# Kernel optimization log

Hardware: AMD Instinct MI355X
Metric: run time of the kernel (lower is better)

## Reference

```python
import jax, jax.numpy as jnp
import numpy as np

N_NODES = 100000
N_EDGES = 1600000
IN_FEATS = 16
HIDDEN = 100
OUT_FEATS = 3


def setup_inputs() -> dict:
    key = jax.random.key(0)
    ks = jax.random.split(key, 12)
    inp = {
        "x": jax.random.normal(ks[0], (N_NODES, IN_FEATS), dtype=jnp.float32),
        "edge_feats": jax.random.uniform(ks[1], (N_EDGES, 1), dtype=jnp.float32),
        "src": jax.random.randint(ks[2], (N_EDGES,), 0, N_NODES, dtype=jnp.int32),
        "dst": jax.random.randint(ks[3], (N_EDGES,), 0, N_NODES, dtype=jnp.int32),
        # lift: Linear(in_feats, hidden)
        "W_lift": jax.random.normal(ks[4], (IN_FEATS, HIDDEN), dtype=jnp.float32) / np.sqrt(IN_FEATS),
        "b_lift": jnp.zeros((HIDDEN,), dtype=jnp.float32),
        # three MPL layers: Linear(2*hidden, hidden)
        "W1": jax.random.normal(ks[5], (2 * HIDDEN, HIDDEN), dtype=jnp.float32) / np.sqrt(2 * HIDDEN),
        "b1": jnp.zeros((HIDDEN,), dtype=jnp.float32),
        "W2": jax.random.normal(ks[6], (2 * HIDDEN, HIDDEN), dtype=jnp.float32) / np.sqrt(2 * HIDDEN),
        "b2": jnp.zeros((HIDDEN,), dtype=jnp.float32),
        "W3": jax.random.normal(ks[7], (2 * HIDDEN, HIDDEN), dtype=jnp.float32) / np.sqrt(2 * HIDDEN),
        "b3": jnp.zeros((HIDDEN,), dtype=jnp.float32),
        # out: Linear(hidden, out_feats)
        "W_out": jax.random.normal(ks[8], (HIDDEN, OUT_FEATS), dtype=jnp.float32) / np.sqrt(HIDDEN),
        "b_out": jnp.zeros((OUT_FEATS,), dtype=jnp.float32),
    }
    return inp


def _mpl(h, edge_feats, src, dst, W, b):
    # gather src node feats, multiply by per-edge weight, scatter-sum to dst
    msg = h[src] * edge_feats                                # [E, H]
    reduced = jax.ops.segment_sum(msg, dst, num_segments=N_NODES)  # [N, H]
    return jax.nn.relu(jnp.concatenate([h, reduced], axis=-1) @ W + b)


def reference(x, edge_feats, src, dst, W_lift, b_lift, W1, b1, W2, b2, W3, b3, W_out, b_out):
    h = jnp.tanh(x @ W_lift + b_lift)          # [N, 100]
    h = _mpl(h, edge_feats, src, dst, W1, b1)
    h = _mpl(h, edge_feats, src, dst, W2, b2)
    h = _mpl(h, edge_feats, src, dst, W3, b3)
    return jax.nn.sigmoid(h @ W_out + b_out)   # [N, 3]
```

## Files before the change

kernel.cpp:

```cpp
#include <hip/hip_runtime.h>
#include <hip/hip_fp16.h>
#include <cstdint>
#include <cstddef>

#define NN 100000
#define NE 1600000
#define HID 100
#define INF 16

typedef _Float16 f16x8 __attribute__((ext_vector_type(8)));
typedef float f32x4 __attribute__((ext_vector_type(4)));

__device__ __forceinline__ float2 up_f16(unsigned int u) {
  __half2 h = *reinterpret_cast<const __half2*>(&u);
  return __half22float2(h);
}
__device__ __forceinline__ unsigned int pk_f16(float lo, float hi) {
  __half2 h = __floats2half2_rn(lo, hi);
  return *reinterpret_cast<const unsigned int*>(&h);
}
__device__ __forceinline__ f16x8 as_f16x8(uint4 v) {
  union { uint4 u; f16x8 f; } c; c.u = v; return c.f;
}

__global__ void k_hist(const int* __restrict__ dst, int* __restrict__ deg,
                       int* __restrict__ rank) {
  int e = blockIdx.x * 256 + threadIdx.x;
  if (e < NE) rank[e] = atomicAdd(&deg[dst[e]], 1);
}

__global__ void k_scan1(const int* __restrict__ deg, int* __restrict__ offs,
                        int* __restrict__ bsum) {
  __shared__ int s[256];
  int t = threadIdx.x;
  int i = blockIdx.x * 256 + t;
  int v = (i < NN) ? deg[i] : 0;
  s[t] = v; __syncthreads();
  for (int off = 1; off < 256; off <<= 1) {
    int x = (t >= off) ? s[t - off] : 0;
    __syncthreads();
    s[t] += x;
    __syncthreads();
  }
  if (i < NN) offs[i] = s[t] - v;
  if (t == 255) bsum[blockIdx.x] = s[255];
}

__global__ void k_scan2(int* __restrict__ bsum, int nb) {
  __shared__ int s[512];
  int t = threadIdx.x;
  int v = (t < nb) ? bsum[t] : 0;
  s[t] = v; __syncthreads();
  for (int off = 1; off < 512; off <<= 1) {
    int x = (t >= off) ? s[t - off] : 0;
    __syncthreads();
    s[t] += x;
    __syncthreads();
  }
  if (t < nb) bsum[t] = s[t] - v;
}

__global__ void k_scan3(int* __restrict__ offs, const int* __restrict__ bsum) {
  int i = blockIdx.x * 256 + threadIdx.x;
  if (i < NN) offs[i] += bsum[i >> 8];
  else if (i == NN) offs[NN] = NE;
}

__global__ void k_fill(const int* __restrict__ src, const int* __restrict__ dst,
                       const float* __restrict__ ef, const int* __restrict__ offs,
                       const int* __restrict__ rank,
                       unsigned long long* __restrict__ epack) {
  int e = blockIdx.x * 256 + threadIdx.x;
  if (e >= NE) return;
  int p = offs[dst[e]] + rank[e];
  unsigned long long v = (unsigned int)src[e] |
                         ((unsigned long long)(unsigned int)__float_as_int(ef[e]) << 32);
  epack[p] = v;
}

__device__ __forceinline__ float wval(const float* W, int kp, int col) {
  if (col >= HID) return 0.f;
  if (kp < 128) return (kp < 100) ? W[kp * HID + col] : 0.f;
  int k2 = kp - 128;
  return (k2 < 100) ? W[(100 + k2) * HID + col] : 0.f;
}
__global__ void k_wpack(const float* __restrict__ W, uint4* __restrict__ Bp) {
  int tid = blockIdx.x * 256 + threadIdx.x;
  if (tid >= 56 * 64) return;
  int lane = tid & 63, f = tid >> 6;
  int s = f / 7, n = f % 7;
  int col = n * 16 + (lane & 15);
  int kb = s * 32 + (lane >> 4) * 8;
  unsigned int u0 = pk_f16(wval(W, kb + 0, col), wval(W, kb + 1, col));
  unsigned int u1 = pk_f16(wval(W, kb + 2, col), wval(W, kb + 3, col));
  unsigned int u2 = pk_f16(wval(W, kb + 4, col), wval(W, kb + 5, col));
  unsigned int u3 = pk_f16(wval(W, kb + 6, col), wval(W, kb + 7, col));
  Bp[tid] = make_uint4(u0, u1, u2, u3);
}

__global__ __launch_bounds__(256) void k_lift(const float* __restrict__ x,
                                              const float* __restrict__ Wl,
                                              const float* __restrict__ bl,
                                              unsigned short* __restrict__ h16) {
  int n = blockIdx.x * 256 + threadIdx.x;
  if (n >= NN) return;
  const float4* W4 = (const float4*)Wl;
  const float4* b4 = (const float4*)bl;
  float4 acc[25];
  #pragma unroll
  for (int j = 0; j < 25; ++j) acc[j] = b4[j];
  const float4* xr = (const float4*)(x + (size_t)n * INF);
  for (int k4 = 0; k4 < 4; ++k4) {
    float4 xv = xr[k4];
    #pragma unroll
    for (int c = 0; c < 4; ++c) {
      float xs = (&xv.x)[c];
      int k = k4 * 4 + c;
      #pragma unroll
      for (int j = 0; j < 25; ++j) {
        acc[j].x = fmaf(xs, W4[k * 25 + j].x, acc[j].x);
        acc[j].y = fmaf(xs, W4[k * 25 + j].y, acc[j].y);
        acc[j].z = fmaf(xs, W4[k * 25 + j].z, acc[j].z);
        acc[j].w = fmaf(xs, W4[k * 25 + j].w, acc[j].w);
      }
    }
  }
  uint2* o = (uint2*)(h16 + (size_t)n * HID);
  #pragma unroll
  for (int j = 0; j < 25; ++j) {
    float4 v = acc[j];
    o[j] = make_uint2(pk_f16(tanhf(v.x), tanhf(v.y)),
                      pk_f16(tanhf(v.z), tanhf(v.w)));
  }
}

__global__ __launch_bounds__(256) void k_reduce(const unsigned short* __restrict__ h16,
                                                const int* __restrict__ offs,
                                                const int2* __restrict__ ep,
                                                unsigned int* __restrict__ red16) {
  int wid = (blockIdx.x * 256 + threadIdx.x) >> 6;
  int node = __builtin_amdgcn_readfirstlane(wid);
  int lane = threadIdx.x & 63;
  int lc = lane < 25 ? lane : 24;
  int beg = offs[node], end = offs[node + 1];
  const uint2* __restrict__ h2 = (const uint2*)h16;
  float4 acc = make_float4(0.f, 0.f, 0.f, 0.f);
  int i = beg;
  for (; i + 4 <= end; i += 4) {
    int2 e0 = ep[i + 0], e1 = ep[i + 1], e2 = ep[i + 2], e3 = ep[i + 3];
    uint2 v0 = h2[(size_t)e0.x * 25 + lc];
    uint2 v1 = h2[(size_t)e1.x * 25 + lc];
    uint2 v2 = h2[(size_t)e2.x * 25 + lc];
    uint2 v3 = h2[(size_t)e3.x * 25 + lc];
    float w0 = __int_as_float(e0.y), w1 = __int_as_float(e1.y);
    float w2 = __int_as_float(e2.y), w3 = __int_as_float(e3.y);
    float2 a0 = up_f16(v0.x), b0 = up_f16(v0.y);
    float2 a1 = up_f16(v1.x), b1 = up_f16(v1.y);
    float2 a2 = up_f16(v2.x), b2 = up_f16(v2.y);
    float2 a3 = up_f16(v3.x), b3 = up_f16(v3.y);
    acc.x = fmaf(w0, a0.x, acc.x); acc.y = fmaf(w0, a0.y, acc.y);
    acc.z = fmaf(w0, b0.x, acc.z); acc.w = fmaf(w0, b0.y, acc.w);
    acc.x = fmaf(w1, a1.x, acc.x); acc.y = fmaf(w1, a1.y, acc.y);
    acc.z = fmaf(w1, b1.x, acc.z); acc.w = fmaf(w1, b1.y, acc.w);
    acc.x = fmaf(w2, a2.x, acc.x); acc.y = fmaf(w2, a2.y, acc.y);
    acc.z = fmaf(w2, b2.x, acc.z); acc.w = fmaf(w2, b2.y, acc.w);
    acc.x = fmaf(w3, a3.x, acc.x); acc.y = fmaf(w3, a3.y, acc.y);
    acc.z = fmaf(w3, b3.x, acc.z); acc.w = fmaf(w3, b3.y, acc.w);
  }
  for (; i < end; ++i) {
    int2 e0 = ep[i];
    uint2 v0 = h2[(size_t)e0.x * 25 + lc];
    float w0 = __int_as_float(e0.y);
    float2 a0 = up_f16(v0.x), b0 = up_f16(v0.y);
    acc.x = fmaf(w0, a0.x, acc.x); acc.y = fmaf(w0, a0.y, acc.y);
    acc.z = fmaf(w0, b0.x, acc.z); acc.w = fmaf(w0, b0.y, acc.w);
  }
  if (lane < 25) {
    ((uint2*)red16)[(size_t)node * 25 + lane] =
        make_uint2(pk_f16(acc.x, acc.y), pk_f16(acc.z, acc.w));
  }
}

__global__ __launch_bounds__(256) void k_mlp(const unsigned int* __restrict__ hp,
                                             const unsigned int* __restrict__ rp,
                                             const uint4* __restrict__ Bpk,
                                             const float* __restrict__ bias,
                                             unsigned short* __restrict__ out16) {
  __shared__ unsigned int xs[64 * 132];
  const int t = threadIdx.x;
  const int w = t >> 6, lane = t & 63;
  const int blk = blockIdx.x;
  const size_t base2 = (size_t)blk * 3200;
  const size_t limit2 = (size_t)NN * 50;

  for (int i = t; i < 64 * 28; i += 256) {
    int row = i / 28, c = i % 28;
    int col = (c < 14) ? (50 + c) : (100 + c);
    xs[row * 132 + col] = 0;
  }
  for (int i = t; i < 3200; i += 256) {
    int row = i / 50, c = i % 50;
    size_t g = base2 + i; if (g >= limit2) g = limit2 - 1;
    xs[row * 132 + c] = hp[g];
    xs[row * 132 + 64 + c] = rp[g];
  }
  __syncthreads();

  const int rowA = (w << 4) + (lane & 15);
  const int kg = lane >> 4;
  f32x4 acc[7];
  #pragma unroll
  for (int n = 0; n < 7; ++n) {
    int c = n * 16 + (lane & 15);
    float bv = (c < HID) ? bias[c] : 0.f;
    acc[n] = (f32x4){bv, bv, bv, bv};
  }
  const uint4* bp = Bpk + lane;
  #pragma unroll
  for (int s = 0; s < 8; ++s) {
    uint4 av = *reinterpret_cast<const uint4*>(&xs[rowA * 132 + s * 16 + kg * 4]);
    f16x8 af = as_f16x8(av);
    #pragma unroll
    for (int n = 0; n < 7; ++n) {
      f16x8 bf = as_f16x8(bp[(s * 7 + n) * 64]);
      acc[n] = __builtin_amdgcn_mfma_f32_16x16x32_f16(af, bf, acc[n], 0, 0, 0);
    }
  }
  const int orow0 = blk * 64 + (w << 4) + (kg << 2);
  const int ocol = lane & 15;
  #pragma unroll
  for (int n = 0; n < 7; ++n) {
    int c = n * 16 + ocol;
    if (c < HID) {
      #pragma unroll
      for (int q = 0; q < 4; ++q) {
        int rr = orow0 + q;
        if (rr < NN) {
          float v = fmaxf(acc[n][q], 0.f);
          out16[(size_t)rr * HID + c] = __half_as_ushort(__float2half(v));
        }
      }
    }
  }
}

__global__ __launch_bounds__(256) void k_out(const unsigned short* __restrict__ h16,
                                             const float* __restrict__ Wo,
                                             const float* __restrict__ bo,
                                             float* __restrict__ out) {
  int n = blockIdx.x * 256 + threadIdx.x;
  if (n >= NN) return;
  float a0 = bo[0], a1 = bo[1], a2 = bo[2];
  const uint2* hr = (const uint2*)(h16 + (size_t)n * HID);
  for (int k2 = 0; k2 < 25; ++k2) {
    uint2 v = hr[k2];
    float2 fa = up_f16(v.x), fb = up_f16(v.y);
    int k = k2 * 4;
    a0 = fmaf(fa.x, Wo[(k + 0) * 3 + 0], a0); a1 = fmaf(fa.x, Wo[(k + 0) * 3 + 1], a1); a2 = fmaf(fa.x, Wo[(k + 0) * 3 + 2], a2);
    a0 = fmaf(fa.y, Wo[(k + 1) * 3 + 0], a0); a1 = fmaf(fa.y, Wo[(k + 1) * 3 + 1], a1); a2 = fmaf(fa.y, Wo[(k + 1) * 3 + 2], a2);
    a0 = fmaf(fb.x, Wo[(k + 2) * 3 + 0], a0); a1 = fmaf(fb.x, Wo[(k + 2) * 3 + 1], a1); a2 = fmaf(fb.x, Wo[(k + 2) * 3 + 2], a2);
    a0 = fmaf(fb.y, Wo[(k + 3) * 3 + 0], a0); a1 = fmaf(fb.y, Wo[(k + 3) * 3 + 1], a1); a2 = fmaf(fb.y, Wo[(k + 3) * 3 + 2], a2);
  }
  out[(size_t)n * 3 + 0] = 1.f / (1.f + expf(-a0));
  out[(size_t)n * 3 + 1] = 1.f / (1.f + expf(-a1));
  out[(size_t)n * 3 + 2] = 1.f / (1.f + expf(-a2));
}

extern "C" void kernel_launch(void* const* d_in, const int* in_sizes, int n_in,
                              void* d_out, int out_size, void* d_ws, size_t ws_size,
                              hipStream_t stream) {
  const float* x  = (const float*)d_in[0];
  const float* ef = (const float*)d_in[1];
  const int*   src = (const int*)d_in[2];
  const int*   dst = (const int*)d_in[3];
  const float* Wl = (const float*)d_in[4];
  const float* bl = (const float*)d_in[5];
  const float* W1 = (const float*)d_in[6];
  const float* b1 = (const float*)d_in[7];
  const float* W2 = (const float*)d_in[8];
  const float* b2 = (const float*)d_in[9];
  const float* W3 = (const float*)d_in[10];
  const float* b3 = (const float*)d_in[11];
  const float* Wo = (const float*)d_in[12];
  const float* bo = (const float*)d_in[13];
  float* out = (float*)d_out;

  char* ws = (char*)d_ws;
  unsigned int*   red16  = (unsigned int*)(ws);
  uint4*          Wpk    = (uint4*)(ws + 20000000);
  unsigned short* hA16   = (unsigned short*)(ws + 40000000);
  unsigned short* hB16   = (unsigned short*)(ws + 60000000);
  int*            offs   = (int*)(ws + 80000000);
  int*            deg    = (int*)(ws + 80400128);
  unsigned long long* epack = (unsigned long long*)(ws + 80800256);
  int*            bsum   = (int*)(ws + 93600256);
  int*            rank   = (int*)red16;

  const int scanBlocks = (NN + 255) / 256;
  const int mlpBlocks  = (NN + 63) / 64;
  uint4* Wpk1 = Wpk;
  uint4* Wpk2 = Wpk + 3584;
  uint4* Wpk3 = Wpk + 7168;

  hipMemsetAsync(deg, 0, NN * sizeof(int), stream);
  k_hist <<<(NE + 255) / 256, 256, 0, stream>>>(dst, deg, rank);
  k_scan1<<<scanBlocks, 256, 0, stream>>>(deg, offs, bsum);
  k_scan2<<<1, 512, 0, stream>>>(bsum, scanBlocks);
  k_scan3<<<scanBlocks, 256, 0, stream>>>(offs, bsum);
  k_fill <<<(NE + 255) / 256, 256, 0, stream>>>(src, dst, ef, offs, rank, epack);

  k_wpack<<<14, 256, 0, stream>>>(W1, Wpk1);
  k_wpack<<<14, 256, 0, stream>>>(W2, Wpk2);
  k_wpack<<<14, 256, 0, stream>>>(W3, Wpk3);

  k_lift<<<scanBlocks, 256, 0, stream>>>(x, Wl, bl, hA16);

  k_reduce<<<NN / 4, 256, 0, stream>>>(hA16, offs, (const int2*)epack, red16);
  k_mlp   <<<mlpBlocks, 256, 0, stream>>>((const unsigned int*)hA16, red16, Wpk1, b1, hB16);

  k_reduce<<<NN / 4, 256, 0, stream>>>(hB16, offs, (const int2*)epack, red16);
  k_mlp   <<<mlpBlocks, 256, 0, stream>>>((const unsigned int*)hB16, red16, Wpk2, b2, hA16);

  k_reduce<<<NN / 4, 256, 0, stream>>>(hA16, offs, (const int2*)epack, red16);
  k_mlp   <<<mlpBlocks, 256, 0, stream>>>((const unsigned int*)hA16, red16, Wpk3, b3, hB16);

  k_out<<<scanBlocks, 256, 0, stream>>>(hB16, Wo, bo, out);
}
```

Baseline: 518.7 us.

## Privatize degree histogram into 8 copies and coalesce lift output via LDS

The degree histogram now spreads atomics over 8 per-block-group copies, so fewer atomics contend on the same counter. A new kernel sums the copies into per-group prefix offsets, which the fill step uses to place edges in CSR order. Separately, the lift kernel stages its fp16 output in shared memory and writes it out with coalesced 16-byte stores instead of strided per-thread rows. This costs an extra kernel, a larger memset and more workspace traffic, and the lift kernel now uses a sizable LDS buffer.

```diff
diff --git a/kernel.cpp b/kernel.cpp
--- a/kernel.cpp
+++ b/kernel.cpp
@@ -7,6 +7,7 @@
 #define NE 1600000
 #define HID 100
 #define INF 16
+#define NP 100096
 
 typedef _Float16 f16x8 __attribute__((ext_vector_type(8)));
 typedef float f32x4 __attribute__((ext_vector_type(4)));
@@ -23,10 +24,26 @@
   union { uint4 u; f16x8 f; } c; c.u = v; return c.f;
 }
 
-__global__ void k_hist(const int* __restrict__ dst, int* __restrict__ deg,
+__global__ void k_hist(const int* __restrict__ dst, int* __restrict__ deg8,
                        int* __restrict__ rank) {
   int e = blockIdx.x * 256 + threadIdx.x;
-  if (e < NE) rank[e] = atomicAdd(&deg[dst[e]], 1);
+  if (e >= NE) return;
+  int g = blockIdx.x & 7;
+  rank[e] = atomicAdd(&deg8[g * NP + dst[e]], 1);
+}
+
+__global__ void k_sumdeg(const int* __restrict__ deg8, int* __restrict__ gpre,
+                         int* __restrict__ deg) {
+  int n = blockIdx.x * 256 + threadIdx.x;
+  if (n >= NN) return;
+  int run = 0;
+  #pragma unroll
+  for (int g = 0; g < 8; ++g) {
+    int t = deg8[g * NP + n];
+    gpre[g * NP + n] = run;
+    run += t;
+  }
+  deg[n] = run;
 }
 
 __global__ void k_scan1(const int* __restrict__ deg, int* __restrict__ offs,
@@ -68,11 +85,13 @@
 
 __global__ void k_fill(const int* __restrict__ src, const int* __restrict__ dst,
                        const float* __restrict__ ef, const int* __restrict__ offs,
-                       const int* __restrict__ rank,
+                       const int* __restrict__ gpre, const int* __restrict__ rank,
                        unsigned long long* __restrict__ epack) {
   int e = blockIdx.x * 256 + threadIdx.x;
   if (e >= NE) return;
-  int p = offs[dst[e]] + rank[e];
+  int g = blockIdx.x & 7;
+  int d = dst[e];
+  int p = offs[d] + gpre[g * NP + d] + rank[e];
   unsigned long long v = (unsigned int)src[e] |
                          ((unsigned long long)(unsigned int)__float_as_int(ef[e]) << 32);
   epack[p] = v;
@@ -102,14 +121,16 @@
                                               const float* __restrict__ Wl,
                                               const float* __restrict__ bl,
                                               unsigned short* __restrict__ h16) {
-  int n = blockIdx.x * 256 + threadIdx.x;
-  if (n >= NN) return;
+  __shared__ uint2 sh[256][25];
+  int t = threadIdx.x;
+  int n = blockIdx.x * 256 + t;
+  int nc = n < NN ? n : NN - 1;
   const float4* W4 = (const float4*)Wl;
   const float4* b4 = (const float4*)bl;
   float4 acc[25];
   #pragma unroll
   for (int j = 0; j < 25; ++j) acc[j] = b4[j];
-  const float4* xr = (const float4*)(x + (size_t)n * INF);
+  const float4* xr = (const float4*)(x + (size_t)nc * INF);
   for (int k4 = 0; k4 < 4; ++k4) {
     float4 xv = xr[k4];
     #pragma unroll
@@ -125,12 +146,20 @@
       }
     }
   }
-  uint2* o = (uint2*)(h16 + (size_t)n * HID);
   #pragma unroll
   for (int j = 0; j < 25; ++j) {
     float4 v = acc[j];
-    o[j] = make_uint2(pk_f16(tanhf(v.x), tanhf(v.y)),
-                      pk_f16(tanhf(v.z), tanhf(v.w)));
+    sh[t][j] = make_uint2(pk_f16(tanhf(v.x), tanhf(v.y)),
+                          pk_f16(tanhf(v.z), tanhf(v.w)));
+  }
+  __syncthreads();
+  const uint4* shv = (const uint4*)sh;
+  uint4* ov = (uint4*)h16;
+  size_t gbase = (size_t)blockIdx.x * 3200;
+  #pragma unroll
+  for (int i = 0; i < 13; ++i) {
+    int idx = i * 256 + t;
+    if (idx < 3200 && gbase + idx < 1250000) ov[gbase + idx] = shv[idx];
   }
 }
 
@@ -294,7 +323,9 @@
   int*            deg    = (int*)(ws + 80400128);
   unsigned long long* epack = (unsigned long long*)(ws + 80800256);
   int*            bsum   = (int*)(ws + 93600256);
-  int*            rank   = (int*)red16;
+  int*            rank   = (int*)ws;
+  int*            deg8   = (int*)(ws + 6400000);
+  int*            gpre   = (int*)(ws + 9603072);
 
   const int scanBlocks = (NN + 255) / 256;
   const int mlpBlocks  = (NN + 63) / 64;
@@ -302,12 +333,13 @@
   uint4* Wpk2 = Wpk + 3584;
   uint4* Wpk3 = Wpk + 7168;
 
-  hipMemsetAsync(deg, 0, NN * sizeof(int), stream);
-  k_hist <<<(NE + 255) / 256, 256, 0, stream>>>(dst, deg, rank);
-  k_scan1<<<scanBlocks, 256, 0, stream>>>(deg, offs, bsum);
-  k_scan2<<<1, 512, 0, stream>>>(bsum, scanBlocks);
-  k_scan3<<<scanBlocks, 256, 0, stream>>>(offs, bsum);
-  k_fill <<<(NE + 255) / 256, 256, 0, stream>>>(src, dst, ef, offs, rank, epack);
+  hipMemsetAsync(deg8, 0, 8 * NP * sizeof(int), stream);
+  k_hist  <<<(NE + 255) / 256, 256, 0, stream>>>(dst, deg8, rank);
+  k_sumdeg<<<scanBlocks, 256, 0, stream>>>(deg8, gpre, deg);
+  k_scan1 <<<scanBlocks, 256, 0, stream>>>(deg, offs, bsum);
+  k_scan2 <<<1, 512, 0, stream>>>(bsum, scanBlocks);
+  k_scan3 <<<scanBlocks, 256, 0, stream>>>(offs, bsum);
+  k_fill  <<<(NE + 255) / 256, 256, 0, stream>>>(src, dst, ef, offs, gpre, rank, epack);
 
   k_wpack<<<14, 256, 0, stream>>>(W1, Wpk1);
   k_wpack<<<14, 256, 0, stream>>>(W2, Wpk2);
```

Measured after the change: 522.1 us. No clear change (+0.7%).
